# Kernel tuning notes

Measured on AMD Instinct MI355X. Metric: run time of the kernel, lower is better.

Reference implementation:

```python
import jax, jax.numpy as jnp
import numpy as np

D_MODEL, D_FF, D_KEY, D_VALUE, NUM_HEADS = 1024, 4096, 64, 64, 16
EPS = 1e-5
B, S = 2, 2048


def layer_norm(x, gamma, beta):
    # torch x.var() default is unbiased (ddof=1)
    mean = jnp.mean(x, axis=-1, keepdims=True)
    var = jnp.var(x, axis=-1, keepdims=True, ddof=1)
    return (x - mean) / jnp.sqrt(var + EPS) * gamma + beta


def setup_inputs() -> dict:
    key = jax.random.key(0)
    ks = jax.random.split(key, 16)
    s = 0.02
    return {
        "x": jax.random.normal(ks[0], (B, S, D_MODEL), dtype=jnp.float32),
        "mask": jnp.zeros((B, 1, 1, S), dtype=bool),
        "Wq": jax.random.normal(ks[1], (D_MODEL, NUM_HEADS * D_KEY), dtype=jnp.float32) * s,
        "bq": jnp.zeros((NUM_HEADS * D_KEY,), jnp.float32),
        "Wk": jax.random.normal(ks[2], (D_MODEL, NUM_HEADS * D_KEY), dtype=jnp.float32) * s,
        "bk": jnp.zeros((NUM_HEADS * D_KEY,), jnp.float32),
        "Wv": jax.random.normal(ks[3], (D_MODEL, NUM_HEADS * D_VALUE), dtype=jnp.float32) * s,
        "bv": jnp.zeros((NUM_HEADS * D_VALUE,), jnp.float32),
        "Wo": jax.random.normal(ks[4], (NUM_HEADS * D_VALUE, D_MODEL), dtype=jnp.float32) * s,
        "bo": jnp.zeros((D_MODEL,), jnp.float32),
        "gamma1": jnp.ones((D_MODEL,), jnp.float32),
        "beta1": jnp.zeros((D_MODEL,), jnp.float32),
        "W1": jax.random.normal(ks[5], (D_MODEL, D_FF), dtype=jnp.float32) * s,
        "b1": jnp.zeros((D_FF,), jnp.float32),
        "W2": jax.random.normal(ks[6], (D_FF, D_MODEL), dtype=jnp.float32) * s,
        "b2": jnp.zeros((D_MODEL,), jnp.float32),
        "gamma2": jnp.ones((D_MODEL,), jnp.float32),
        "beta2": jnp.zeros((D_MODEL,), jnp.float32),
    }


def reference(x, mask, Wq, bq, Wk, bk, Wv, bv, Wo, bo, gamma1, beta1, W1, b1, W2, b2, gamma2, beta2):
    Bsz, Sq, _ = x.shape
    # ---- multi-head attention (self-attention) ----
    q = (x @ Wq + bq).reshape(Bsz, Sq, NUM_HEADS, D_KEY)
    k = (x @ Wk + bk).reshape(Bsz, Sq, NUM_HEADS, D_KEY)
    v = (x @ Wv + bv).reshape(Bsz, Sq, NUM_HEADS, D_VALUE)
    scores = jnp.einsum("bqhd,bkhd->bhqk", q, k) / jnp.sqrt(jnp.float32(D_KEY))
    scores = jnp.where(mask, -jnp.inf, scores)
    attn = jax.nn.softmax(scores, axis=-1)
    ctx = jnp.einsum("bhqk,bkhd->bqhd", attn, v).reshape(Bsz, Sq, NUM_HEADS * D_VALUE)
    attn_out = ctx @ Wo + bo
    # ---- residual + LN, FFN, residual + LN ----
    h = layer_norm(attn_out + x, gamma1, beta1)
    ff = jnp.maximum(h @ W1 + b1, 0.0) @ W2 + b2
    out = layer_norm(ff + h, gamma2, beta2)
    return out
```

## Files before the change

kernel.cpp:

```cpp
#include <hip/hip_runtime.h>
#include <cstddef>
#include <cstdint>

#define BATCH   2
#define SEQ     2048
#define DMODEL  1024
#define DFF     4096
#define NHEADS  16
#define DHEAD   64
#define NTOK    (BATCH * SEQ)
#define LN_EPS  1e-5f

typedef __attribute__((ext_vector_type(8))) short bf16x8;
typedef __attribute__((ext_vector_type(4))) float f32x4;

#define MFMA(a, b, c) __builtin_amdgcn_mfma_f32_16x16x32_bf16((a), (b), (c), 0, 0, 0)

__device__ __forceinline__ unsigned short f2bf(float f) {
    unsigned int u = __float_as_uint(f);
    u += 0x7fffu + ((u >> 16) & 1u);
    return (unsigned short)(u >> 16);
}

__device__ __forceinline__ void gld_lds16(const void* g, void* l) {
    __builtin_amdgcn_global_load_lds(
        (const __attribute__((address_space(1))) void*)g,
        (__attribute__((address_space(3))) void*)l, 16, 0, 0);
}

template <int MODE>
__global__ __launch_bounds__(512, 2) void gemm256(
    const short* __restrict__ A, const short* __restrict__ Bt,
    const float* __restrict__ bias, unsigned short* __restrict__ C0,
    unsigned short* __restrict__ C1, int M, int N, int K)
{
    __shared__ __align__(16) short As[4][256][32];
    __shared__ __align__(16) short Bs[4][256][32];

    const int tid  = threadIdx.x;
    const int lane = tid & 63;
    const int w    = tid >> 6;
    const int wm   = w >> 2;
    const int wn   = w & 3;
    const int row0 = blockIdx.y * 256;
    const int col0 = blockIdx.x * 256;
    const int m    = lane & 15;
    const int qd   = lane >> 4;

    f32x4 acc[8][4] = {};

    const short* gAs = A  + (size_t)(row0 + w * 32 + (lane >> 2)) * K + (lane & 3) * 8;
    const short* gBs = Bt + (size_t)(col0 + w * 32 + (lane >> 2)) * K + (lane & 3) * 8;

    const int NT = K >> 5;

#define STAGE32(sl, s) do {                                                 \
    const size_t ko = (size_t)(s) << 5;                                     \
    gld_lds16(gAs + ko,                  &As[sl][w * 32][0]);               \
    gld_lds16(gAs + (size_t)16 * K + ko, &As[sl][w * 32 + 16][0]);          \
    gld_lds16(gBs + ko,                  &Bs[sl][w * 32][0]);               \
    gld_lds16(gBs + (size_t)16 * K + ko, &Bs[sl][w * 32 + 16][0]);          \
} while (0)

    STAGE32(0, 0);
    if (NT > 1) STAGE32(1, 1);
    if (NT > 2) STAGE32(2, 2);

    for (int s = 0; s < NT; ++s) {
        const int slot = s & 3;
        if (s + 2 < NT)      asm volatile("s_waitcnt vmcnt(8)" ::: "memory");
        else if (s + 1 < NT) asm volatile("s_waitcnt vmcnt(4)" ::: "memory");
        else                 asm volatile("s_waitcnt vmcnt(0)" ::: "memory");
        __builtin_amdgcn_s_barrier();
        asm volatile("" ::: "memory");
        if (s + 3 < NT) STAGE32((s + 3) & 3, s + 3);

        const short (*Al)[32] = As[slot];
        const short (*Bl)[32] = Bs[slot];

        bf16x8 bfr[4];
#pragma unroll
        for (int ni = 0; ni < 4; ++ni)
            bfr[ni] = *(const bf16x8*)&Bl[wn * 64 + ni * 16 + m][qd * 8];

        bf16x8 afr[4];
#pragma unroll
        for (int mi = 0; mi < 4; ++mi)
            afr[mi] = *(const bf16x8*)&Al[wm * 128 + mi * 16 + m][qd * 8];
        __builtin_amdgcn_s_setprio(1);
#pragma unroll
        for (int mi = 0; mi < 4; ++mi)
#pragma unroll
            for (int ni = 0; ni < 4; ++ni)
                acc[mi][ni] = MFMA(afr[mi], bfr[ni], acc[mi][ni]);
        __builtin_amdgcn_s_setprio(0);

#pragma unroll
        for (int mi = 0; mi < 4; ++mi)
            afr[mi] = *(const bf16x8*)&Al[wm * 128 + (4 + mi) * 16 + m][qd * 8];
        __builtin_amdgcn_s_setprio(1);
#pragma unroll
        for (int mi = 0; mi < 4; ++mi)
#pragma unroll
            for (int ni = 0; ni < 4; ++ni)
                acc[4 + mi][ni] = MFMA(afr[mi], bfr[ni], acc[4 + mi][ni]);
        __builtin_amdgcn_s_setprio(0);
        asm volatile("" ::: "memory");
    }
#undef STAGE32

    if (MODE == 0) {
#pragma unroll
        for (int mi = 0; mi < 8; ++mi) {
#pragma unroll
            for (int ni = 0; ni < 4; ++ni) {
                const int col = col0 + wn * 64 + ni * 16 + m;
                const float bv = bias[col];
#pragma unroll
                for (int r = 0; r < 4; ++r) {
                    const int row = row0 + wm * 128 + mi * 16 + qd * 4 + r;
                    float v = fmaxf(acc[mi][ni][r] + bv, 0.0f);
                    C0[(size_t)row * N + col] = f2bf(v);
                }
            }
        }
    } else {
        const int mode = (col0 >= 2048) ? 2 : (col0 < 1024 ? 0 : 1);
        const float scale = (mode == 0) ? 0.1803368801111204f : 1.0f;
#pragma unroll
        for (int mi = 0; mi < 8; ++mi) {
#pragma unroll
            for (int ni = 0; ni < 4; ++ni) {
                const int col = col0 + wn * 64 + ni * 16 + m;
                const float bv = bias[col];
#pragma unroll
                for (int r = 0; r < 4; ++r) {
                    const int row = row0 + wm * 128 + mi * 16 + qd * 4 + r;
                    const float v = (acc[mi][ni][r] + bv) * scale;
                    if (mode < 2) {
                        C0[(size_t)row * 2048 + col] = f2bf(v);
                    } else {
                        const int hd  = col - 2048;
                        const int bb  = row >> 11;
                        const int key = row & (SEQ - 1);
                        C1[((size_t)(bb * 1024 + hd)) * SEQ + key] = f2bf(v);
                    }
                }
            }
        }
    }
}

__global__ __launch_bounds__(256) void gemm_sk64(
    const short* __restrict__ A, const short* __restrict__ Bt,
    const float* __restrict__ bias,
    float* __restrict__ P0, float* __restrict__ P1, int M, int N, int K)
{
    __shared__ __align__(16) short As[128][64];
    __shared__ __align__(16) short Bs[64][64];

    const int tid  = threadIdx.x;
    const int lane = tid & 63;
    const int w    = tid >> 6;
    const int row0 = blockIdx.y * 128;
    const int col0 = blockIdx.x * 64;
    const int z    = blockIdx.z;
    const int KH   = K >> 1;
    const int kofs = z * KH;
    const int wr   = w * 32;
    const int m    = lane & 15;
    const int q    = lane >> 4;

    f32x4 acc[2][4] = {};

    const int cg = (lane & 7) ^ ((lane >> 3) & 7);
    const short* ga = A  + (size_t)(row0 + w * 32 + (lane >> 3)) * K + kofs + cg * 8;
    const short* gb = Bt + (size_t)(col0 + w * 16 + (lane >> 3)) * K + kofs + cg * 8;

    for (int k0 = 0; k0 < KH; k0 += 64) {
#pragma unroll
        for (int i = 0; i < 4; ++i)
            gld_lds16(ga + (size_t)i * 8 * K + k0, &As[w * 32 + i * 8][0]);
#pragma unroll
        for (int i = 0; i < 2; ++i)
            gld_lds16(gb + (size_t)i * 8 * K + k0, &Bs[w * 16 + i * 8][0]);
        __syncthreads();

#pragma unroll
        for (int kk = 0; kk < 2; ++kk) {
            bf16x8 af[2], bfr[4];
#pragma unroll
            for (int i = 0; i < 2; ++i) {
                const int row = wr + i * 16 + m;
                af[i] = *(const bf16x8*)&As[row][((kk * 4 + q) ^ (row & 7)) * 8];
            }
#pragma unroll
            for (int i = 0; i < 4; ++i) {
                const int row = i * 16 + m;
                bfr[i] = *(const bf16x8*)&Bs[row][((kk * 4 + q) ^ (row & 7)) * 8];
            }
#pragma unroll
            for (int mi = 0; mi < 2; ++mi)
#pragma unroll
                for (int ni = 0; ni < 4; ++ni)
                    acc[mi][ni] = MFMA(af[mi], bfr[ni], acc[mi][ni]);
        }
        __syncthreads();
    }

    float* dst = z ? P1 : P0;
    const float bscale = z ? 0.0f : 1.0f;
#pragma unroll
    for (int mi = 0; mi < 2; ++mi) {
#pragma unroll
        for (int ni = 0; ni < 4; ++ni) {
            const int col = col0 + ni * 16 + m;
            const float bv = bias[col] * bscale;
#pragma unroll
            for (int r = 0; r < 4; ++r) {
                const int row = row0 + wr + mi * 16 + q * 4 + r;
                dst[(size_t)row * N + col] = acc[mi][ni][r] + bv;
            }
        }
    }
}

__global__ __launch_bounds__(256, 2) void attn_mfma(
    const short* __restrict__ Qp,
    const short* __restrict__ Kp,
    const short* __restrict__ Vtg,
    float* __restrict__ PO0, float* __restrict__ PO1,
    float* __restrict__ lbuf)
{
    __shared__ __align__(16) short Ks[2][64][64];
    __shared__ __align__(16) short Vs[2][64][64];
    __shared__ __align__(16) short Ps[4][64][64];

    const int tid  = threadIdx.x;
    const int lane = tid & 63;
    const int w    = tid >> 6;
    const int kv   = blockIdx.x & 1;
    const int q0   = (blockIdx.x >> 1) * 256;
    const int h    = blockIdx.y;
    const int b    = blockIdx.z;
    const int m    = lane & 15;
    const int qd   = lane >> 4;
    const int j0   = kv * 16;

    bf16x8 qreg[4][2];
#pragma unroll
    for (int g = 0; g < 4; ++g) {
        const short* gq = Qp + (size_t)(b * SEQ + q0 + w * 64 + g * 16 + m) * 2048 + h * 64;
        qreg[g][0] = *(const bf16x8*)(gq + qd * 8);
        qreg[g][1] = *(const bf16x8*)(gq + (qd + 4) * 8);
    }

    bf16x8 bones;
#pragma unroll
    for (int c = 0; c < 8; ++c) bones[c] = (short)0x3F80;

    const int cg = (lane & 7) ^ (lane >> 3);
    const short* Kg = Kp  + (size_t)(b * SEQ) * 2048 + h * 64 + cg * 8;
    const short* Vg = Vtg + (size_t)(b * 1024 + h * 64) * SEQ + cg * 8;

    {
        const short* gk = Kg + (size_t)(j0 * 64 + w * 16 + (lane >> 3)) * 2048;
        gld_lds16(gk,            &Ks[0][w * 16][0]);
        gld_lds16(gk + 8 * 2048, &Ks[0][w * 16 + 8][0]);
        const short* gv = Vg + (size_t)(w * 16 + (lane >> 3)) * SEQ + j0 * 64;
        gld_lds16(gv,            &Vs[0][w * 16][0]);
        gld_lds16(gv + 8 * SEQ,  &Vs[0][w * 16 + 8][0]);
    }

    f32x4 lacc[4] = {};
    f32x4 oacc[4][4] = {};

    for (int jj = 0; jj < 16; ++jj) {
        const int j   = j0 + jj;
        const int cur = jj & 1;
        __syncthreads();
        if (jj + 1 < 16) {
            const int nb = 1 - cur;
            const short* gk = Kg + (size_t)((j + 1) * 64 + w * 16 + (lane >> 3)) * 2048;
            gld_lds16(gk,            &Ks[nb][w * 16][0]);
            gld_lds16(gk + 8 * 2048, &Ks[nb][w * 16 + 8][0]);
            const short* gv = Vg + (size_t)(w * 16 + (lane >> 3)) * SEQ + (j + 1) * 64;
            gld_lds16(gv,            &Vs[nb][w * 16][0]);
            gld_lds16(gv + 8 * SEQ,  &Vs[nb][w * 16 + 8][0]);
        }

        bf16x8 bkf[2][4];
#pragma unroll
        for (int ks = 0; ks < 2; ++ks)
#pragma unroll
            for (int ni = 0; ni < 4; ++ni) {
                const int kn = ni * 16 + m;
                bkf[ks][ni] = *(const bf16x8*)&Ks[cur][kn][((ks * 4 + qd) ^ (kn & 7)) * 8];
            }

#pragma unroll
        for (int g = 0; g < 4; ++g) {
            f32x4 sacc[4] = {};
#pragma unroll
            for (int ks = 0; ks < 2; ++ks)
#pragma unroll
                for (int ni = 0; ni < 4; ++ni)
                    sacc[ni] = MFMA(qreg[g][ks], bkf[ks][ni], sacc[ni]);
#pragma unroll
            for (int ni = 0; ni < 4; ++ni)
#pragma unroll
                for (int r = 0; r < 4; ++r) {
                    const float p = __builtin_amdgcn_exp2f(sacc[ni][r]);
                    const int row = g * 16 + qd * 4 + r;
                    const int swc = (ni * 2 + (m >> 3)) ^ (row & 7);
                    Ps[w][row][swc * 8 + (m & 7)] = (short)(__float_as_uint(p) >> 16);
                }
        }

        bf16x8 bvf[2][4];
#pragma unroll
        for (int ks = 0; ks < 2; ++ks)
#pragma unroll
            for (int ni = 0; ni < 4; ++ni) {
                const int dn = ni * 16 + m;
                bvf[ks][ni] = *(const bf16x8*)&Vs[cur][dn][((ks * 4 + qd) ^ (dn & 7)) * 8];
            }

#pragma unroll
        for (int g = 0; g < 4; ++g) {
#pragma unroll
            for (int ks = 0; ks < 2; ++ks) {
                bf16x8 ap = *(const bf16x8*)&Ps[w][g * 16 + m][((ks * 4 + qd) ^ (m & 7)) * 8];
                lacc[g] = MFMA(ap, bones, lacc[g]);
#pragma unroll
                for (int ni = 0; ni < 4; ++ni)
                    oacc[g][ni] = MFMA(ap, bvf[ks][ni], oacc[g][ni]);
            }
        }
    }

    float* dst = kv ? PO1 : PO0;
#pragma unroll
    for (int g = 0; g < 4; ++g) {
#pragma unroll
        for (int ni = 0; ni < 4; ++ni)
#pragma unroll
            for (int r = 0; r < 4; ++r) {
                const int row = q0 + w * 64 + g * 16 + qd * 4 + r;
                const int col = h * 64 + ni * 16 + m;
                dst[(size_t)(b * SEQ + row) * DMODEL + col] = oacc[g][ni][r];
            }
        if (m == 0) {
#pragma unroll
            for (int r = 0; r < 4; ++r) {
                const int row = q0 + w * 64 + g * 16 + qd * 4 + r;
                lbuf[(((size_t)kv * BATCH + b) * NHEADS + h) * SEQ + row] = lacc[g][r];
            }
        }
    }
}

__global__ __launch_bounds__(256) void attn_comb(
    const float* __restrict__ PO0, const float* __restrict__ PO1,
    const float* __restrict__ lbuf, unsigned short* __restrict__ CTX)
{
    const int row = blockIdx.x;
    const int tid = threadIdx.x;
    const int b   = row >> 11;
    const int s   = row & (SEQ - 1);
    const int h   = tid >> 4;

    const float l0 = lbuf[(((size_t)0 * BATCH + b) * NHEADS + h) * SEQ + s];
    const float l1 = lbuf[(((size_t)1 * BATCH + b) * NHEADS + h) * SEQ + s];
    const float inv = 1.0f / (l0 + l1);

    const float4 o0 = ((const float4*)(PO0 + (size_t)row * DMODEL))[tid];
    const float4 o1 = ((const float4*)(PO1 + (size_t)row * DMODEL))[tid];
    short4 o;
    o.x = (short)f2bf((o0.x + o1.x) * inv);
    o.y = (short)f2bf((o0.y + o1.y) * inv);
    o.z = (short)f2bf((o0.z + o1.z) * inv);
    o.w = (short)f2bf((o0.w + o1.w) * inv);
    *(short4*)((short*)CTX + (size_t)row * DMODEL + tid * 4) = o;
}

__global__ __launch_bounds__(256) void prep(
    const float* __restrict__ x,
    const float* __restrict__ Wq, const float* __restrict__ Wk,
    const float* __restrict__ Wv, const float* __restrict__ Wo,
    const float* __restrict__ W1, const float* __restrict__ W2,
    const float* __restrict__ bq, const float* __restrict__ bk,
    const float* __restrict__ bv,
    short* __restrict__ xb, short* __restrict__ Wqkvt, short* __restrict__ Wot,
    short* __restrict__ W1t, short* __restrict__ W2t, float* __restrict__ bqkv)
{
    __shared__ float t[32][33];
    const int id  = blockIdx.x;
    const int tid = threadIdx.x;

    if (id < 4096) {
        const size_t i = ((size_t)id * 256 + tid) * 4;
        const float4 v = *(const float4*)(x + i);
        short4 o;
        o.x = (short)f2bf(v.x); o.y = (short)f2bf(v.y);
        o.z = (short)f2bf(v.z); o.w = (short)f2bf(v.w);
        *(short4*)(xb + i) = o;
        return;
    }
    if (id >= 16384) {
        const int i = (id - 16384) * 256 + tid;
        bqkv[i] = (i < 1024) ? bq[i] : (i < 2048 ? bk[i - 1024] : bv[i - 2048]);
        return;
    }

    const float* W; short* Wt; int K, N, bx, by;
    if (id < 8192) {
        const int i2 = id - 4096;
        W = W1; Wt = W1t; K = 1024; N = 4096;
        bx = (i2 & 127) * 32; by = (i2 >> 7) * 32;
    } else if (id < 12288) {
        const int i2 = id - 8192;
        W = W2; Wt = W2t; K = 4096; N = 1024;
        bx = (i2 & 31) * 32; by = (i2 >> 5) * 32;
    } else {
        const int i2 = id - 12288;
        const int z = i2 >> 10, i3 = i2 & 1023;
        W  = (z == 0) ? Wq : (z == 1) ? Wk : (z == 2) ? Wv : Wo;
        Wt = (z == 3) ? Wot : (Wqkvt + (size_t)z * 1024 * 1024);
        K = 1024; N = 1024;
        bx = (i3 & 31) * 32; by = (i3 >> 5) * 32;
    }
    const int c = tid & 31, r8 = tid >> 5;
#pragma unroll
    for (int i = 0; i < 4; ++i)
        t[r8 + i * 8][c] = W[(size_t)(by + r8 + i * 8) * N + bx + c];
    __syncthreads();
#pragma unroll
    for (int i = 0; i < 4; ++i)
        Wt[(size_t)(bx + r8 + i * 8) * K + by + c] = (short)f2bf(t[c][r8 + i * 8]);
}

template <bool BF16OUT>
__global__ __launch_bounds__(256) void ln_comb(
    const float* __restrict__ P0, const float* __restrict__ P1,
    const float* __restrict__ res,
    const float* __restrict__ gamma, const float* __restrict__ beta,
    float* __restrict__ Y, short* __restrict__ Yb)
{
    const int row = blockIdx.x;
    const int tid = threadIdx.x;
    __shared__ float red[256];

    const float4 p0 = ((const float4*)(P0  + (size_t)row * DMODEL))[tid];
    const float4 p1 = ((const float4*)(P1  + (size_t)row * DMODEL))[tid];
    const float4 rv = ((const float4*)(res + (size_t)row * DMODEL))[tid];
    float4 xv;
    xv.x = p0.x + p1.x + rv.x;
    xv.y = p0.y + p1.y + rv.y;
    xv.z = p0.z + p1.z + rv.z;
    xv.w = p0.w + p1.w + rv.w;

    red[tid] = xv.x + xv.y + xv.z + xv.w;
    __syncthreads();
    for (int st = 128; st > 0; st >>= 1) {
        if (tid < st) red[tid] += red[tid + st];
        __syncthreads();
    }
    const float mean = red[0] / (float)DMODEL;
    __syncthreads();

    const float dx0 = xv.x - mean, dx1 = xv.y - mean;
    const float dx2 = xv.z - mean, dx3 = xv.w - mean;
    red[tid] = dx0 * dx0 + dx1 * dx1 + dx2 * dx2 + dx3 * dx3;
    __syncthreads();
    for (int st = 128; st > 0; st >>= 1) {
        if (tid < st) red[tid] += red[tid + st];
        __syncthreads();
    }
    const float var = red[0] / (float)(DMODEL - 1);
    const float rs = rsqrtf(var + LN_EPS);

    const float4 gv = ((const float4*)gamma)[tid];
    const float4 bv = ((const float4*)beta)[tid];
    float4 o;
    o.x = dx0 * rs * gv.x + bv.x;
    o.y = dx1 * rs * gv.y + bv.y;
    o.z = dx2 * rs * gv.z + bv.z;
    o.w = dx3 * rs * gv.w + bv.w;
    ((float4*)(Y + (size_t)row * DMODEL))[tid] = o;
    if (BF16OUT) {
        short4 ob;
        ob.x = (short)f2bf(o.x); ob.y = (short)f2bf(o.y);
        ob.z = (short)f2bf(o.z); ob.w = (short)f2bf(o.w);
        *(short4*)(Yb + (size_t)row * DMODEL + tid * 4) = ob;
    }
}

extern "C" void kernel_launch(void* const* d_in, const int* in_sizes, int n_in,
                              void* d_out, int out_size, void* d_ws, size_t ws_size,
                              hipStream_t stream)
{
    const float* x   = (const float*)d_in[0];
    const float* Wq  = (const float*)d_in[2];
    const float* bq  = (const float*)d_in[3];
    const float* Wk  = (const float*)d_in[4];
    const float* bk  = (const float*)d_in[5];
    const float* Wv  = (const float*)d_in[6];
    const float* bv  = (const float*)d_in[7];
    const float* Wo  = (const float*)d_in[8];
    const float* bo  = (const float*)d_in[9];
    const float* g1  = (const float*)d_in[10];
    const float* be1 = (const float*)d_in[11];
    const float* W1  = (const float*)d_in[12];
    const float* b1  = (const float*)d_in[13];
    const float* W2  = (const float*)d_in[14];
    const float* b2  = (const float*)d_in[15];
    const float* g2  = (const float*)d_in[16];
    const float* be2 = (const float*)d_in[17];
    float* out = (float*)d_out;
    char*  ws  = (char*)d_ws;
    (void)in_sizes; (void)n_in; (void)out_size; (void)ws_size;

    const size_t MB = 1ull << 20;
    short* xb    = (short*)(ws);
    short* W1t   = (short*)(ws + 8 * MB);
    short* W2t   = (short*)(ws + 16 * MB);
    short* Wqkvt = (short*)(ws + 24 * MB);
    short* Wot   = (short*)(ws + 30 * MB);
    float* bqkv  = (float*)(ws + 32 * MB);
    float* lbuf  = (float*)(ws + 32 * MB + 64 * 1024);
    short* QKb   = (short*)(ws + 33 * MB);
    unsigned short* Vtg = (unsigned short*)(ws + 49 * MB);
    unsigned short* CTX = (unsigned short*)(ws + 57 * MB);
    float* PO0   = (float*)(ws + 65 * MB);
    float* PA0   = (float*)(ws + 33 * MB);
    float* hF    = (float*)(ws + 33 * MB);
    short* Hb    = (short*)(ws);
    float* PF0   = (float*)(ws);
    short* F1    = (short*)(ws + 49 * MB);

    dim3 blk(256);

    prep<<<dim3(16396), blk, 0, stream>>>(x, Wq, Wk, Wv, Wo, W1, W2, bq, bk, bv,
                                          xb, Wqkvt, Wot, W1t, W2t, bqkv);

    gemm256<1><<<dim3(3072 / 256, NTOK / 256), dim3(512), 0, stream>>>(
        xb, Wqkvt, bqkv, (unsigned short*)QKb, Vtg, NTOK, 3072, DMODEL);

    attn_mfma<<<dim3((SEQ / 256) * 2, NHEADS, BATCH), blk, 0, stream>>>(
        QKb, QKb + 1024, (const short*)Vtg, PO0, out, lbuf);
    attn_comb<<<dim3(NTOK), blk, 0, stream>>>(PO0, out, lbuf, CTX);

    gemm_sk64<<<dim3(DMODEL / 64, NTOK / 128, 2), blk, 0, stream>>>(
        (const short*)CTX, Wot, bo, PA0, out, NTOK, DMODEL, DMODEL);
    ln_comb<true><<<NTOK, blk, 0, stream>>>(PA0, out, x, g1, be1, hF, Hb);

    gemm256<0><<<dim3(DFF / 256, NTOK / 256), dim3(512), 0, stream>>>(
        Hb, W1t, b1, (unsigned short*)F1, nullptr, NTOK, DFF, DMODEL);

    gemm_sk64<<<dim3(DMODEL / 64, NTOK / 128, 2), blk, 0, stream>>>(
        F1, W2t, b2, PF0, out, NTOK, DMODEL, DFF);
    ln_comb<false><<<NTOK, blk, 0, stream>>>(PF0, out, hF, g2, be2, out, nullptr);
}
```

Before: 394.6 us.

## Swizzle LDS chunks in GEMM tiles and split A/B prefetch staging

Applies an XOR swizzle to the 16-byte chunk index when copying A and B tiles from global memory into LDS, and uses the matching swizzled offset when reading fragments, so that MFMA fragment reads hit fewer LDS bank conflicts. The staging is also restructured: each wave now loads rows w*16 and 128+w*16, B is prefetched two stages ahead and A three stages ahead. The A prefetch is issued in the middle of the MFMA sequence and the vmcnt waits are adjusted to match. The intent is to cut LDS read stalls and spread global-load issue across the compute. This adds risk in the waitcnt accounting and the slot reuse across the four LDS buffers.

```diff
diff --git a/kernel.cpp b/kernel.cpp
--- a/kernel.cpp
+++ b/kernel.cpp
@@ -34,8 +34,8 @@
     const float* __restrict__ bias, unsigned short* __restrict__ C0,
     unsigned short* __restrict__ C1, int M, int N, int K)
 {
-    __shared__ __align__(16) short As[4][256][32];
-    __shared__ __align__(16) short Bs[4][256][32];
+    __shared__ __align__(16) short As4[4][256][32];
+    __shared__ __align__(16) short Bs4[4][256][32];
 
     const int tid  = threadIdx.x;
     const int lane = tid & 63;
@@ -49,44 +49,42 @@
 
     f32x4 acc[8][4] = {};
 
-    const short* gAs = A  + (size_t)(row0 + w * 32 + (lane >> 2)) * K + (lane & 3) * 8;
-    const short* gBs = Bt + (size_t)(col0 + w * 32 + (lane >> 2)) * K + (lane & 3) * 8;
-
-    const int NT = K >> 5;
-
-#define STAGE32(sl, s) do {                                                 \
-    const size_t ko = (size_t)(s) << 5;                                     \
-    gld_lds16(gAs + ko,                  &As[sl][w * 32][0]);               \
-    gld_lds16(gAs + (size_t)16 * K + ko, &As[sl][w * 32 + 16][0]);          \
-    gld_lds16(gBs + ko,                  &Bs[sl][w * 32][0]);               \
-    gld_lds16(gBs + (size_t)16 * K + ko, &Bs[sl][w * 32 + 16][0]);          \
+    const short* gA = A  + (size_t)(row0 + w * 16 + (lane >> 2)) * K
+                         + ((lane & 3) ^ ((lane >> 3) & 3)) * 8;
+    const short* gB = Bt + (size_t)(col0 + w * 16 + (lane >> 2)) * K
+                         + ((lane & 3) ^ ((lane >> 3) & 3)) * 8;
+
+    const int NS = K >> 5;
+
+#define STAGE_A(sj) do { const size_t ko = (size_t)(sj) << 5;               \
+    gld_lds16(gA + ko,                   &As4[(sj) & 3][w * 16][0]);        \
+    gld_lds16(gA + (size_t)128 * K + ko, &As4[(sj) & 3][128 + w * 16][0]);  \
 } while (0)
-
-    STAGE32(0, 0);
-    if (NT > 1) STAGE32(1, 1);
-    if (NT > 2) STAGE32(2, 2);
-
-    for (int s = 0; s < NT; ++s) {
+#define STAGE_B(sj) do { const size_t ko = (size_t)(sj) << 5;               \
+    gld_lds16(gB + ko,                   &Bs4[(sj) & 3][w * 16][0]);        \
+    gld_lds16(gB + (size_t)128 * K + ko, &Bs4[(sj) & 3][128 + w * 16][0]);  \
+} while (0)
+
+    STAGE_A(0); STAGE_B(0); STAGE_A(1); STAGE_B(1); STAGE_A(2);
+
+    const int rchk = (qd ^ ((m >> 1) & 3)) * 8;
+
+    for (int s = 0; s < NS; ++s) {
         const int slot = s & 3;
-        if (s + 2 < NT)      asm volatile("s_waitcnt vmcnt(8)" ::: "memory");
-        else if (s + 1 < NT) asm volatile("s_waitcnt vmcnt(4)" ::: "memory");
-        else                 asm volatile("s_waitcnt vmcnt(0)" ::: "memory");
+        if (s <= NS - 3)      asm volatile("s_waitcnt vmcnt(6)" ::: "memory");
+        else if (s == NS - 2) asm volatile("s_waitcnt vmcnt(4)" ::: "memory");
+        else                  asm volatile("s_waitcnt vmcnt(0)" ::: "memory");
         __builtin_amdgcn_s_barrier();
         asm volatile("" ::: "memory");
-        if (s + 3 < NT) STAGE32((s + 3) & 3, s + 3);
-
-        const short (*Al)[32] = As[slot];
-        const short (*Bl)[32] = Bs[slot];
-
-        bf16x8 bfr[4];
+
+        if (s + 2 < NS) STAGE_B(s + 2);
+        bf16x8 bfr[4], afr[4];
 #pragma unroll
         for (int ni = 0; ni < 4; ++ni)
-            bfr[ni] = *(const bf16x8*)&Bl[wn * 64 + ni * 16 + m][qd * 8];
-
-        bf16x8 afr[4];
+            bfr[ni] = *(const bf16x8*)&Bs4[slot][wn * 64 + ni * 16 + m][rchk];
 #pragma unroll
         for (int mi = 0; mi < 4; ++mi)
-            afr[mi] = *(const bf16x8*)&Al[wm * 128 + mi * 16 + m][qd * 8];
+            afr[mi] = *(const bf16x8*)&As4[slot][wm * 128 + mi * 16 + m][rchk];
         __builtin_amdgcn_s_setprio(1);
 #pragma unroll
         for (int mi = 0; mi < 4; ++mi)
@@ -95,9 +93,10 @@
                 acc[mi][ni] = MFMA(afr[mi], bfr[ni], acc[mi][ni]);
         __builtin_amdgcn_s_setprio(0);
 
+        if (s + 3 < NS) STAGE_A(s + 3);
 #pragma unroll
         for (int mi = 0; mi < 4; ++mi)
-            afr[mi] = *(const bf16x8*)&Al[wm * 128 + (4 + mi) * 16 + m][qd * 8];
+            afr[mi] = *(const bf16x8*)&As4[slot][wm * 128 + (4 + mi) * 16 + m][rchk];
         __builtin_amdgcn_s_setprio(1);
 #pragma unroll
         for (int mi = 0; mi < 4; ++mi)
@@ -107,7 +106,8 @@
         __builtin_amdgcn_s_setprio(0);
         asm volatile("" ::: "memory");
     }
-#undef STAGE32
+#undef STAGE_A
+#undef STAGE_B
 
     if (MODE == 0) {
 #pragma unroll
```

After: 399.5 us. About the same (+1.2%).
